# Optimization experiments

Hardware: AMD Instinct MI355X
Metric: run time of the kernel (lower is better)

## Reference

```python
import jax, jax.numpy as jnp
import numpy as np

N = 50000      # nodes
E = 800000     # edges (avg degree 16)
IN = 128       # input feature dim
D = 128        # embed dim (heads=1, concat)
SLOPE = 0.2    # GATv2Conv default negative_slope


def setup_inputs() -> dict:
    key = jax.random.key(0)
    ks = jax.random.split(key, 16)
    s_in = 1.0 / np.sqrt(IN)
    s_d = 1.0 / np.sqrt(D)
    inp = {
        "node_fts": jax.random.normal(ks[0], (N, IN), dtype=jnp.float32),
        "edge_index": jax.random.randint(ks[1], (2, E), 0, N, dtype=jnp.int64),
        # layer 1 (in_dim -> embed_dim)
        "Wl1": jax.random.normal(ks[2], (IN, D), dtype=jnp.float32) * s_in,
        "bl1": jnp.zeros((D,), dtype=jnp.float32),
        "Wr1": jax.random.normal(ks[3], (IN, D), dtype=jnp.float32) * s_in,
        "br1": jnp.zeros((D,), dtype=jnp.float32),
        "att1": jax.random.normal(ks[4], (D,), dtype=jnp.float32) * s_d,
        "bias1": jnp.zeros((D,), dtype=jnp.float32),
        # layer 2 (embed_dim -> embed_dim)
        "Wl2": jax.random.normal(ks[5], (D, D), dtype=jnp.float32) * s_d,
        "bl2": jnp.zeros((D,), dtype=jnp.float32),
        "Wr2": jax.random.normal(ks[6], (D, D), dtype=jnp.float32) * s_d,
        "br2": jnp.zeros((D,), dtype=jnp.float32),
        "att2": jax.random.normal(ks[7], (D,), dtype=jnp.float32) * s_d,
        "bias2": jnp.zeros((D,), dtype=jnp.float32),
    }
    return inp


def gatv2_layer(x, src, dst, Wl, bl, Wr, br, att, bias):
    # GATv2Conv (heads=1, share_weights=False):
    #   x_j (source message features) = lin_l(x), x_i (target) = lin_r(x)
    xl = x @ Wl + bl                                      # [N, D]
    xr = x @ Wr + br                                      # [N, D]
    e = jax.nn.leaky_relu(xl[src] + xr[dst], SLOPE)       # [E, D]
    logits = e @ att                                      # [E]
    # softmax over incoming edges of each target node
    m = jax.ops.segment_max(logits, dst, num_segments=N)  # [N], -inf for isolated
    m = jnp.where(jnp.isneginf(m), 0.0, m)
    a = jnp.exp(logits - m[dst])                          # [E]
    s = jax.ops.segment_sum(a, dst, num_segments=N)       # [N]
    a = a / jnp.maximum(s[dst], 1e-16)
    out = jax.ops.segment_sum(a[:, None] * xl[src], dst, num_segments=N)  # [N, D]
    return out + bias


def reference(node_fts, edge_index,
              Wl1, bl1, Wr1, br1, att1, bias1,
              Wl2, bl2, Wr2, br2, att2, bias2):
    src, dst = edge_index[0], edge_index[1]
    x = jax.nn.relu(gatv2_layer(node_fts, src, dst, Wl1, bl1, Wr1, br1, att1, bias1))
    x = jax.nn.relu(gatv2_layer(x, src, dst, Wl2, bl2, Wr2, br2, att2, bias2))
    return x
```

## Files before the change

### kernel.cpp

```cpp
#include <hip/hip_runtime.h>
#include <hip/hip_bf16.h>
#include <hip/hip_fp16.h>

#define N_NODES 50000
#define N_EDGES 800000
#define DIM 128
#define NGROUPS (N_NODES / 16)
#define LROW2 132
#define KBUCKET 196
#define BCAP 5120
#define EPB 2000
#define OSTR 260

typedef __attribute__((ext_vector_type(8))) _Float16 hfrag8;
typedef __attribute__((ext_vector_type(4))) float f32x4;
typedef _Float16 h2 __attribute__((ext_vector_type(2)));

__device__ __forceinline__ h2 u2h(uint u){ union{uint u; h2 h;} c; c.u = u; return c.h; }

__device__ __forceinline__ float rowsum16(float p) {
  union { float f; int i; } a, b;
  a.f = p;
  b.i = __builtin_amdgcn_update_dpp(0, a.i, 0x128, 0xF, 0xF, true); a.f += b.f;
  b.i = __builtin_amdgcn_update_dpp(0, a.i, 0x124, 0xF, 0xF, true); a.f += b.f;
  b.i = __builtin_amdgcn_update_dpp(0, a.i, 0x122, 0xF, 0xF, true); a.f += b.f;
  b.i = __builtin_amdgcn_update_dpp(0, a.i, 0x121, 0xF, 0xF, true); a.f += b.f;
  return a.f;
}


__global__ __launch_bounds__(256) void bucket_scatter_k(
    const int* __restrict__ src, const int* __restrict__ dst,
    int* __restrict__ bucket_cnt, uint* __restrict__ bucketdata)
{
  __shared__ int cnt[KBUCKET], base[KBUCKET], cur[KBUCKET];
  int tid = threadIdx.x;
  for (int t = tid; t < KBUCKET; t += 256) { cnt[t] = 0; cur[t] = 0; }
  __syncthreads();
  int e0 = blockIdx.x * EPB;
  int dreg[8];
  #pragma unroll
  for (int it = 0; it < 8; it++) {
    int i = it*256 + tid;
    dreg[it] = (i < EPB) ? dst[e0 + i] : -1;
    if (i < EPB) atomicAdd(&cnt[dreg[it] >> 8], 1);
  }
  __syncthreads();
  for (int t = tid; t < KBUCKET; t += 256)
    base[t] = atomicAdd(&bucket_cnt[t], cnt[t]);
  __syncthreads();
  #pragma unroll
  for (int it = 0; it < 8; it++) {
    int i = it*256 + tid;
    if (i < EPB) {
      int s = src[e0 + i], d = dreg[it];
      int b = d >> 8;
      int r = atomicAdd(&cur[b], 1);
      bucketdata[(size_t)b * BCAP + base[b] + r] = ((uint)s << 8) | (uint)(d & 255);
    }
  }
}

__global__ __launch_bounds__(64) void prep_w(
    const float* __restrict__ Wl1, const float* __restrict__ Wr1,
    const float* __restrict__ Wl2, const float* __restrict__ Wr2,
    _Float16* __restrict__ wb, int* __restrict__ bucket_cnt)
{
  int bid = blockIdx.x;
  if (bid == 0) {
    for (int t = threadIdx.x; t < KBUCKET; t += 64) bucket_cnt[t] = 0;
  }
  int layer = bid >> 6, rest = bid & 63;
  int C = rest >> 4, g = rest & 15;
  int lane = threadIdx.x;
  int m = lane & 15, q = lane >> 4;
  int dim = g*16 + m;
  const float* W = layer ? (dim < 128 ? Wl2 : Wr2) : (dim < 128 ? Wl1 : Wr1);
  int dcol = dim & 127;
  _Float16 h[8];
  #pragma unroll
  for (int j = 0; j < 8; j++) {
    int k = C*32 + q*8 + j;
    h[j] = (_Float16)W[(size_t)k*DIM + dcol];
  }
  size_t off = ((size_t)bid*64 + lane)*8;
  *(hfrag8*)(wb + off) = *(hfrag8*)h;
}

__global__ __launch_bounds__(256) void gemm1_csr_k(
    const float* __restrict__ x, const _Float16* __restrict__ wb,
    const float* __restrict__ bl, const float* __restrict__ br,
    __half* __restrict__ xlh, __half* __restrict__ xrh,
    const int* __restrict__ bucket_cnt, const uint* __restrict__ bucketdata,
    int* __restrict__ row_start, int* __restrict__ csr_soff)
{
  __shared__ float lds[4][16*LROW2];
  __shared__ int hist[256], cur[256];
  __shared__ int wsumA[4], wsumB[4];
  int tid = threadIdx.x;

  if (blockIdx.x < KBUCKET) {
    int b = blockIdx.x;
    int lane = tid & 63, w = tid >> 6;
    int vv = (tid < b) ? bucket_cnt[tid] : 0;
    #pragma unroll
    for (int off = 32; off > 0; off >>= 1) vv += __shfl_xor(vv, off, 64);
    if (lane == 0) wsumA[w] = vv;
    hist[tid] = 0;
    __syncthreads();
    int base_csr = wsumA[0] + wsumA[1] + wsumA[2] + wsumA[3];
    int cnt = bucket_cnt[b];
    int node0 = b << 8;
    const uint* bd = bucketdata + (size_t)b * BCAP;
    for (int i = tid; i < cnt; i += 256)
      atomicAdd(&hist[bd[i] & 255], 1);
    __syncthreads();
    int v = hist[tid];
    int inc = v;
    #pragma unroll
    for (int off = 1; off < 64; off <<= 1) {
      int y = __shfl_up(inc, off, 64);
      if (lane >= off) inc += y;
    }
    if (lane == 63) wsumB[w] = inc;
    __syncthreads();
    int wpre = 0;
    #pragma unroll
    for (int i = 0; i < 4; i++) if (i < w) wpre += wsumB[i];
    int excl = wpre + inc - v;
    int node = node0 + tid;
    if (node < N_NODES) row_start[node] = base_csr + excl;
    if (b == 0 && tid == 0) row_start[N_NODES] = N_EDGES;
    cur[tid] = excl;
    __syncthreads();
    for (int i = tid; i < cnt; i += 256) {
      uint p = bd[i];
      int r = atomicAdd(&cur[p & 255], 1);
      csr_soff[base_csr + r] = (int)(p & 0xFFFFFF00u);
    }
    return;
  }

  int wv = tid >> 6, lane = tid & 63;
  int G = (blockIdx.x - KBUCKET) * 4 + wv;
  if (G >= NGROUPS) return;

  int m = lane & 15, q = lane >> 4;
  const float* xrow = x + (size_t)(G*16 + m)*DIM + q*8;

  f32x4 acc[16];
  #pragma unroll
  for (int g = 0; g < 16; g++) acc[g] = (f32x4)(0.f);

  #pragma unroll 1
  for (int C = 0; C < 4; C++) {
    float v[8];
    *(float4*)(v)     = *(const float4*)(xrow + C*32);
    *(float4*)(v + 4) = *(const float4*)(xrow + C*32 + 4);
    _Float16 hh[8];
    #pragma unroll
    for (int j = 0; j < 8; j++) hh[j] = (_Float16)v[j];
    hfrag8 ah = *(hfrag8*)hh;
    #pragma unroll
    for (int g = 0; g < 16; g++) {
      size_t boff = ((size_t)(C*16 + g)*64 + lane)*8;
      hfrag8 bh = *(const hfrag8*)(wb + boff);
      acc[g] = __builtin_amdgcn_mfma_f32_16x16x32_f16(ah, bh, acc[g], 0, 0, 0);
    }
  }

  float* wlds = lds[wv];
  int dcol = (lane & 31) * 4;
  int rowsel = lane >> 5;
  #pragma unroll
  for (int half = 0; half < 2; half++) {
    #pragma unroll
    for (int g = 0; g < 8; g++) {
      #pragma unroll
      for (int r = 0; r < 4; r++)
        wlds[(q*4 + r)*LROW2 + g*16 + m] = acc[half*8 + g][r];
    }
    const float* B = half ? br : bl;
    ushort* outh = half ? (ushort*)xrh : (ushort*)xlh;
    float4 bv = *(const float4*)(B + dcol);
    #pragma unroll
    for (int it = 0; it < 8; it++) {
      int i = it*2 + rowsel;
      float4 vv2 = *(const float4*)(wlds + i*LROW2 + dcol);
      int node = G*16 + i;
      __half2 h0 = __floats2half2_rn(vv2.x + bv.x, vv2.y + bv.y);
      __half2 h1 = __floats2half2_rn(vv2.z + bv.z, vv2.w + bv.w);
      uint2 pk = make_uint2(*(uint*)&h0, *(uint*)&h1);
      *(uint2*)(outh + (size_t)node*DIM + dcol) = pk;
    }
  }
}


#define GAT_IDX(OFF, TBASE)                                             \
  do {                                                                  \
    if ((TBASE) < 32) {                                                 \
      int _src = ((TBASE) < 16) ? my0 : my1;                            \
      _Pragma("unroll")                                                 \
      for (int j = 0; j < 4; j++)                                       \
        OFF[j] = __builtin_amdgcn_ds_bpermute(                          \
                     grpb4 + ((((TBASE) + j) & 15) << 2), _src);        \
    } else {                                                            \
      _Pragma("unroll")                                                 \
      for (int j = 0; j < 4; j++)                                       \
        OFF[j] = csr_soff[min(r0 + (TBASE) + j, last)];                 \
    }                                                                   \
  } while (0)

#define GAT_LDR4(OFF, RAW)                                              \
  _Pragma("unroll")                                                     \
  for (int j = 0; j < 4; j++)                                           \
    RAW[j] = *(const uint4*)(xb + (size_t)(uint)OFF[j]);

#define GAT_BODY(RAW, WEXPR)                                            \
  _Pragma("unroll")                                                     \
  for (int j = 0; j < 4; j++) {                                         \
    h2 v01 = u2h(RAW[j].x), v23 = u2h(RAW[j].y);                        \
    h2 v45 = u2h(RAW[j].z), v67 = u2h(RAW[j].w);                        \
    h2 s01 = v01 + xr01, s23 = v23 + xr23;                              \
    h2 s45 = v45 + xr45, s67 = v67 + xr67;                              \
    s01 = __builtin_elementwise_max(s01, s01 * c02);                    \
    s23 = __builtin_elementwise_max(s23, s23 * c02);                    \
    s45 = __builtin_elementwise_max(s45, s45 * c02);                    \
    s67 = __builtin_elementwise_max(s67, s67 * c02);                    \
    float pA = __builtin_amdgcn_fdot2(s01, a01, 0.f, false);            \
    pA = __builtin_amdgcn_fdot2(s23, a23, pA, false);                   \
    float pB = __builtin_amdgcn_fdot2(s45, a45, 0.f, false);            \
    pB = __builtin_amdgcn_fdot2(s67, a67, pB, false);                   \
    float p = rowsum16(pA + pB);                                        \
    float w = (WEXPR);                                                  \
    l += w;                                                             \
    b0a = fmaf(w, (float)v01.x, b0a); b1a = fmaf(w, (float)v01.y, b1a); \
    b2a = fmaf(w, (float)v23.x, b2a); b3a = fmaf(w, (float)v23.y, b3a); \
    b4a = fmaf(w, (float)v45.x, b4a); b5a = fmaf(w, (float)v45.y, b5a); \
    b6a = fmaf(w, (float)v67.x, b6a); b7a = fmaf(w, (float)v67.y, b7a); \
  }

__device__ __forceinline__ void gather_core(
    int node, int lane,
    const __half* __restrict__ xlh, const __half* __restrict__ xrh,
    const int* __restrict__ row_start, const int* __restrict__ csr_soff,
    const float* __restrict__ att, const float* __restrict__ bias,
    float4& o0, float4& o1)
{
  int hl = lane & 15;
  int grpb4 = (lane & 48) << 2;
  int r0 = row_start[node];
  int deg = row_start[node + 1] - r0;
  int last = r0 + deg - 1;

  int my0 = 0, my1 = 0;
  if (deg > 0) {
    my0 = csr_soff[min(r0 + hl,      last)];
    my1 = csr_soff[min(r0 + 16 + hl, last)];
  }

  uint4 rx = *(const uint4*)((const ushort*)xrh + (size_t)node*DIM + hl*8);
  h2 xr01 = u2h(rx.x), xr23 = u2h(rx.y), xr45 = u2h(rx.z), xr67 = u2h(rx.w);
  const float* ap = att + hl*8;
  float4 af0 = *(const float4*)(ap);
  float4 af1 = *(const float4*)(ap + 4);
  const float L2E = 1.44269504088896f;
  h2 a01 = {(_Float16)(af0.x*L2E), (_Float16)(af0.y*L2E)};
  h2 a23 = {(_Float16)(af0.z*L2E), (_Float16)(af0.w*L2E)};
  h2 a45 = {(_Float16)(af1.x*L2E), (_Float16)(af1.y*L2E)};
  h2 a67 = {(_Float16)(af1.z*L2E), (_Float16)(af1.w*L2E)};
  const h2 c02 = {(_Float16)0.2f, (_Float16)0.2f};

  float l = 0.f;
  float b0a=0,b1a=0,b2a=0,b3a=0,b4a=0,b5a=0,b6a=0,b7a=0;
  const char* xb = (const char*)xlh + hl*16;

  int offA[4]; uint4 rawA[4];
  int offB[4]; uint4 rawB[4];
  int nfull = deg & ~3;

  if (nfull > 0) { GAT_IDX(offA, 0); GAT_LDR4(offA, rawA); }
  #pragma unroll 1
  for (int t = 0; t < nfull; t += 8) {
    bool hasB = (t + 4 < nfull);
    if (hasB) { GAT_IDX(offB, t + 4); GAT_LDR4(offB, rawB); }
    GAT_BODY(rawA, exp2f(p));
    if (t + 8 < nfull) { GAT_IDX(offA, t + 8); GAT_LDR4(offA, rawA); }
    if (hasB) GAT_BODY(rawB, exp2f(p));
  }
  int rem = deg - nfull;
  if (rem > 0) {
    #pragma unroll
    for (int j = 0; j < 4; j++)
      offA[j] = csr_soff[min(r0 + nfull + j, last)];
    GAT_LDR4(offA, rawA);
    GAT_BODY(rawA, (j < rem) ? exp2f(p) : 0.f);
  }

  float inv = 1.f / fmaxf(l, 1e-16f);
  const float* bp = bias + hl*8;
  float4 c0 = *(const float4*)(bp);
  float4 c1 = *(const float4*)(bp + 4);
  o0.x = fmaxf(fmaf(b0a, inv, c0.x), 0.f);
  o0.y = fmaxf(fmaf(b1a, inv, c0.y), 0.f);
  o0.z = fmaxf(fmaf(b2a, inv, c0.z), 0.f);
  o0.w = fmaxf(fmaf(b3a, inv, c0.w), 0.f);
  o1.x = fmaxf(fmaf(b4a, inv, c1.x), 0.f);
  o1.y = fmaxf(fmaf(b5a, inv, c1.y), 0.f);
  o1.z = fmaxf(fmaf(b6a, inv, c1.z), 0.f);
  o1.w = fmaxf(fmaf(b7a, inv, c1.w), 0.f);
}

__global__ __launch_bounds__(256) void fused_g1_gemm2_k(
    const __half* __restrict__ xlh, const __half* __restrict__ xrh,
    const int* __restrict__ row_start, const int* __restrict__ csr_soff,
    const float* __restrict__ att, const float* __restrict__ bias,
    const _Float16* __restrict__ wb2,
    const float* __restrict__ bl2, const float* __restrict__ br2,
    __half* __restrict__ xlh2, __half* __restrict__ xrh2)
{
  __shared__ ushort xs[16*128];
  __shared__ ushort outs[16*OSTR];
  int tid = threadIdx.x;
  int wv = tid >> 6, lane = tid & 63;
  int q4 = lane >> 4, hl = lane & 15;
  int nl = wv*4 + q4;
  int base = blockIdx.x * 16;

  float4 o0, o1;
  gather_core(base + nl, lane, xlh, xrh, row_start, csr_soff, att, bias, o0, o1);
  __half2 p0 = __floats2half2_rn(o0.x, o0.y);
  __half2 p1 = __floats2half2_rn(o0.z, o0.w);
  __half2 p2 = __floats2half2_rn(o1.x, o1.y);
  __half2 p3 = __floats2half2_rn(o1.z, o1.w);
  uint4 pk = make_uint4(*(uint*)&p0, *(uint*)&p1, *(uint*)&p2, *(uint*)&p3);
  *(uint4*)((char*)xs + nl*256 + ((hl*16) ^ ((nl&7)<<4))) = pk;
  __syncthreads();

  int m = lane & 15, q = lane >> 4;
  f32x4 acc[4];
  #pragma unroll
  for (int g = 0; g < 4; g++) acc[g] = (f32x4)(0.f);
  #pragma unroll
  for (int C = 0; C < 4; C++) {
    hfrag8 ah = *(const hfrag8*)((const char*)xs + m*256 + ((C*64 + q*16) ^ ((m&7)<<4)));
    #pragma unroll
    for (int g = 0; g < 4; g++) {
      int gg = wv*4 + g;
      size_t boff = ((size_t)(C*16 + gg)*64 + lane)*8;
      hfrag8 bh = *(const hfrag8*)(wb2 + boff);
      acc[g] = __builtin_amdgcn_mfma_f32_16x16x32_f16(ah, bh, acc[g], 0, 0, 0);
    }
  }
  #pragma unroll
  for (int g = 0; g < 4; g++) {
    int gg = wv*4 + g;
    int dim = gg*16 + m;
    float bv = (gg < 8) ? bl2[dim] : br2[dim - 128];
    #pragma unroll
    for (int r = 0; r < 4; r++) {
      int row = q*4 + r;
      __half hv = __float2half_rn(acc[g][r] + bv);
      outs[row*OSTR + gg*16 + m] = *(ushort*)&hv;
    }
  }
  __syncthreads();
  #pragma unroll
  for (int p = 0; p < 2; p++) {
    int c = p*256 + tid;
    int row = c >> 5, off = c & 31;
    uint4 v = *(const uint4*)((const char*)outs + row*(OSTR*2) + off*16);
    int nodeo = base + row;
    int d0 = off*8;
    ushort* dstp = (d0 < 128) ? ((ushort*)xlh2 + (size_t)nodeo*DIM + d0)
                              : ((ushort*)xrh2 + (size_t)nodeo*DIM + (d0 - 128));
    *(uint4*)dstp = v;
  }
}

__global__ __launch_bounds__(256) void gat_gather2(
    const __half* __restrict__ xlh, const __half* __restrict__ xrh,
    const int* __restrict__ row_start, const int* __restrict__ csr_soff,
    const float* __restrict__ att, const float* __restrict__ bias,
    float* __restrict__ outf)
{
  int wave = (blockIdx.x * 256 + threadIdx.x) >> 6;
  int lane = threadIdx.x & 63;
  int q4 = lane >> 4;
  int hl = lane & 15;
  int node = wave * 4 + q4;
  float4 o0, o1;
  gather_core(node, lane, xlh, xrh, row_start, csr_soff, att, bias, o0, o1);
  float* op = outf + (size_t)node*DIM + hl*8;
  *(float4*)(op)     = o0;
  *(float4*)(op + 4) = o1;
}

extern "C" void kernel_launch(void* const* d_in, const int* in_sizes, int n_in,
                              void* d_out, int out_size, void* d_ws, size_t ws_size,
                              hipStream_t stream)
{
  const float* node_fts = (const float*)d_in[0];
  const int*  edge_index = (const int*)d_in[1];
  const float* Wl1 = (const float*)d_in[2];
  const float* bl1 = (const float*)d_in[3];
  const float* Wr1 = (const float*)d_in[4];
  const float* br1 = (const float*)d_in[5];
  const float* att1 = (const float*)d_in[6];
  const float* bias1 = (const float*)d_in[7];
  const float* Wl2 = (const float*)d_in[8];
  const float* bl2 = (const float*)d_in[9];
  const float* Wr2 = (const float*)d_in[10];
  const float* br2 = (const float*)d_in[11];
  const float* att2 = (const float*)d_in[12];
  const float* bias2 = (const float*)d_in[13];
  const int* src = edge_index;
  const int* dst = edge_index + N_EDGES;

  char* ws = (char*)d_ws;
  __half* xlh = (__half*)ws;               ws += (size_t)N_NODES*DIM*2;
  __half* xrh = (__half*)ws;               ws += (size_t)N_NODES*DIM*2;
  __half* xlh2 = (__half*)ws;              ws += (size_t)N_NODES*DIM*2;
  __half* xrh2 = (__half*)ws;              ws += (size_t)N_NODES*DIM*2;
  _Float16* wb = (_Float16*)ws;            ws += 2*4*16*64*8*2;
  int* row_start   = (int*)ws;             ws += (N_NODES+1)*4;
  int* csr_soff    = (int*)ws;             ws += (size_t)N_EDGES*4;
  int* bucket_cnt  = (int*)ws;             ws += KBUCKET*4;
  uint* bucketdata = (uint*)ws;            ws += (size_t)KBUCKET*BCAP*4;

  const int W_LAYER = 4*16*64*8;

  int gemm_blocks = (NGROUPS + 3) / 4;
  int gather_blocks = N_NODES / 16;

  prep_w<<<128, 64, 0, stream>>>(Wl1, Wr1, Wl2, Wr2, wb, bucket_cnt);
  bucket_scatter_k<<<N_EDGES/EPB, 256, 0, stream>>>(src, dst, bucket_cnt, bucketdata);
  gemm1_csr_k<<<KBUCKET + gemm_blocks, 256, 0, stream>>>(
      node_fts, wb, bl1, br1, xlh, xrh,
      bucket_cnt, bucketdata, row_start, csr_soff);
  fused_g1_gemm2_k<<<gather_blocks, 256, 0, stream>>>(
      xlh, xrh, row_start, csr_soff, att1, bias1,
      wb + W_LAYER, bl2, br2, xlh2, xrh2);
  gat_gather2<<<gather_blocks, 256, 0, stream>>>(
      xlh2, xrh2, row_start, csr_soff, att2, bias2, (float*)d_out);
}
```

Measured before the change: 217.8 us.

## Stage GEMM weight fragments in LDS and store fp16 outputs via LDS transpose

The projection GEMM now copies each K-chunk of pre-packed fp16 weight fragments into shared memory once per block, so all four waves read it from there instead of each loading it from global memory. Bias add and fp16 conversion move before the LDS transpose, which halves the staging footprint and lets each thread write full 16-byte rows. Waves with no work stay alive so they can take part in the barriers. The gather skips the second index load when the degree is 16 or less. The cost is two block barriers per K-chunk.

```diff
diff --git a/kernel.cpp b/kernel.cpp
--- a/kernel.cpp
+++ b/kernel.cpp
@@ -6,11 +6,11 @@
 #define N_EDGES 800000
 #define DIM 128
 #define NGROUPS (N_NODES / 16)
-#define LROW2 132
 #define KBUCKET 196
 #define BCAP 5120
 #define EPB 2000
 #define OSTR 260
+#define TSTR 132
 
 typedef __attribute__((ext_vector_type(8))) _Float16 hfrag8;
 typedef __attribute__((ext_vector_type(4))) float f32x4;
@@ -94,9 +94,10 @@
     const int* __restrict__ bucket_cnt, const uint* __restrict__ bucketdata,
     int* __restrict__ row_start, int* __restrict__ csr_soff)
 {
-  __shared__ float lds[4][16*LROW2];
   __shared__ int hist[256], cur[256];
   __shared__ int wsumA[4], wsumB[4];
+  __shared__ _Float16 wstage[16*64*8];
+  __shared__ ushort touts[4][16*TSTR];
   int tid = threadIdx.x;
 
   if (blockIdx.x < KBUCKET) {
@@ -143,7 +144,8 @@
 
   int wv = tid >> 6, lane = tid & 63;
   int G = (blockIdx.x - KBUCKET) * 4 + wv;
-  if (G >= NGROUPS) return;
+  bool wvalid = (G < NGROUPS);
+  if (!wvalid) G = NGROUPS - 1;
 
   int m = lane & 15, q = lane >> 4;
   const float* xrow = x + (size_t)(G*16 + m)*DIM + q*8;
@@ -154,6 +156,15 @@
 
   #pragma unroll 1
   for (int C = 0; C < 4; C++) {
+    __syncthreads();
+    {
+      const uint4* srcw = (const uint4*)(wb + (size_t)C*16*64*8);
+      uint4* dstw = (uint4*)wstage;
+      #pragma unroll
+      for (int k = 0; k < 4; k++)
+        dstw[k*256 + tid] = srcw[k*256 + tid];
+    }
+    __syncthreads();
     float v[8];
     *(float4*)(v)     = *(const float4*)(xrow + C*32);
     *(float4*)(v + 4) = *(const float4*)(xrow + C*32 + 4);
@@ -163,35 +174,32 @@
     hfrag8 ah = *(hfrag8*)hh;
     #pragma unroll
     for (int g = 0; g < 16; g++) {
-      size_t boff = ((size_t)(C*16 + g)*64 + lane)*8;
-      hfrag8 bh = *(const hfrag8*)(wb + boff);
+      hfrag8 bh = *(const hfrag8*)(wstage + ((size_t)g*64 + lane)*8);
       acc[g] = __builtin_amdgcn_mfma_f32_16x16x32_f16(ah, bh, acc[g], 0, 0, 0);
     }
   }
 
-  float* wlds = lds[wv];
-  int dcol = (lane & 31) * 4;
-  int rowsel = lane >> 5;
+  ushort* tw = touts[wv];
   #pragma unroll
   for (int half = 0; half < 2; half++) {
-    #pragma unroll
-    for (int g = 0; g < 8; g++) {
-      #pragma unroll
-      for (int r = 0; r < 4; r++)
-        wlds[(q*4 + r)*LROW2 + g*16 + m] = acc[half*8 + g][r];
-    }
     const float* B = half ? br : bl;
     ushort* outh = half ? (ushort*)xrh : (ushort*)xlh;
-    float4 bv = *(const float4*)(B + dcol);
-    #pragma unroll
-    for (int it = 0; it < 8; it++) {
-      int i = it*2 + rowsel;
-      float4 vv2 = *(const float4*)(wlds + i*LROW2 + dcol);
-      int node = G*16 + i;
-      __half2 h0 = __floats2half2_rn(vv2.x + bv.x, vv2.y + bv.y);
-      __half2 h1 = __floats2half2_rn(vv2.z + bv.z, vv2.w + bv.w);
-      uint2 pk = make_uint2(*(uint*)&h0, *(uint*)&h1);
-      *(uint2*)(outh + (size_t)node*DIM + dcol) = pk;
+    #pragma unroll
+    for (int g = 0; g < 8; g++) {
+      float bv = B[g*16 + m];
+      #pragma unroll
+      for (int r = 0; r < 4; r++) {
+        __half hv = __float2half_rn(acc[half*8 + g][r] + bv);
+        tw[(q*4 + r)*TSTR + g*16 + m] = *(ushort*)&hv;
+      }
+    }
+    #pragma unroll
+    for (int i = 0; i < 4; i++) {
+      int c = i*64 + lane;
+      int row = c >> 4, off = c & 15;
+      uint4 vv = *(const uint4*)((const char*)tw + row*(TSTR*2) + off*16);
+      if (wvalid)
+        *(uint4*)(outh + (size_t)(G*16 + row)*DIM + off*8) = vv;
     }
   }
 }
@@ -255,10 +263,8 @@
   int last = r0 + deg - 1;
 
   int my0 = 0, my1 = 0;
-  if (deg > 0) {
-    my0 = csr_soff[min(r0 + hl,      last)];
-    my1 = csr_soff[min(r0 + 16 + hl, last)];
-  }
+  if (deg > 0)  my0 = csr_soff[min(r0 + hl,      last)];
+  if (deg > 16) my1 = csr_soff[min(r0 + 16 + hl, last)];
 
   uint4 rx = *(const uint4*)((const ushort*)xrh + (size_t)node*DIM + hl*8);
   h2 xr01 = u2h(rx.x), xr23 = u2h(rx.y), xr45 = u2h(rx.z), xr67 = u2h(rx.w);
```

Result: no change. 214.7 us (-1.4%).
